# Performance work log

Hardware: AMD Instinct MI355X
Metric: run time of the kernel (lower is better)

## Reference

```python
import jax, jax.numpy as jnp
import numpy as np

N_NODES = 100000
N_EDGES = 1600000
IN_DIM = 64
HID = 64
EDGE_DIM = 1
NUM_GRAPHS = 1000
SCALE = 0.05


def setup_inputs() -> dict:
    key = jax.random.key(0)
    ks = jax.random.split(key, 20)
    x = jax.random.normal(ks[0], (N_NODES, IN_DIM), dtype=jnp.float32)
    edge_index = jax.random.randint(ks[1], (2, N_EDGES), 0, N_NODES, dtype=jnp.int64)
    edge_attr = jax.random.normal(ks[2], (N_EDGES, EDGE_DIM), dtype=jnp.float32)
    batch = jnp.sort(jax.random.randint(ks[3], (N_NODES,), 0, NUM_GRAPHS, dtype=jnp.int64))
    p = lambda k, shp: SCALE * jax.random.normal(k, shp, dtype=jnp.float32)
    return {
        "x": x, "edge_index": edge_index, "edge_attr": edge_attr, "batch": batch,
        # conv1 MLP + edge lin
        "W1a": p(ks[4], (IN_DIM, HID)), "b1a": p(ks[5], (HID,)),
        "W1b": p(ks[6], (HID, HID)), "b1b": p(ks[7], (HID,)),
        "We1": p(ks[8], (EDGE_DIM, IN_DIM)), "be1": p(ks[9], (IN_DIM,)),
        # conv2 MLP + edge lin
        "W2a": p(ks[10], (HID, HID)), "b2a": p(ks[11], (HID,)),
        "W2b": p(ks[12], (HID, HID)), "b2b": p(ks[13], (HID,)),
        "We2": p(ks[14], (EDGE_DIM, HID)), "be2": p(ks[15], (HID,)),
        # classifier
        "Wc1": p(ks[16], (HID, HID)), "bc1": p(ks[17], (HID,)),
        "Wc2": p(ks[18], (HID, 1)), "bc2": p(ks[19], (1,)),
    }


def _gine(x, src, dst, e_proj, Wa, ba, Wb, bb):
    # message: ReLU(x_src + projected edge feature); scatter-sum to target
    msg = jax.nn.relu(x[src] + e_proj)                      # [E, D]
    agg = jax.ops.segment_sum(msg, dst, num_segments=x.shape[0])
    h = x + agg                                             # eps = 0 (default)
    return jax.nn.relu(h @ Wa + ba) @ Wb + bb               # GIN MLP


def reference(x, edge_index, edge_attr, batch,
              W1a, b1a, W1b, b1b, We1, be1,
              W2a, b2a, W2b, b2b, We2, be2,
              Wc1, bc1, Wc2, bc2):
    src, dst = edge_index[0], edge_index[1]
    h = _gine(x, src, dst, edge_attr @ We1 + be1, W1a, b1a, W1b, b1b)
    h = jax.nn.relu(h)  # dropout is identity in eval mode
    h = _gine(h, src, dst, edge_attr @ We2 + be2, W2a, b2a, W2b, b2b)
    h = jax.nn.relu(h)
    # global mean pool over graphs
    sums = jax.ops.segment_sum(h, batch, num_segments=NUM_GRAPHS)
    cnts = jax.ops.segment_sum(jnp.ones((h.shape[0], 1), h.dtype), batch, num_segments=NUM_GRAPHS)
    pooled = sums / jnp.maximum(cnts, 1.0)                  # [G, HID]
    return jax.nn.relu(pooled @ Wc1 + bc1) @ Wc2 + bc2      # [G, 1]
```

## Files before the change

kernel.cpp:

```cpp
#include <hip/hip_runtime.h>

#define N_NODES    100000
#define N_EDGES    1600000
#define DIM        64
#define NUM_GRAPHS 1000
#define CONV_BLK   3125
#define PAD        72

#define SLICES     512
#define SLICE_E    3125
#define NBUCK      782
#define CAP4       3072

typedef __attribute__((ext_vector_type(8))) short bf16x8;
typedef __attribute__((ext_vector_type(4))) float f32x4;

__device__ __forceinline__ unsigned short f2bf(float f) {
    unsigned int b = __float_as_uint(f);
    b += 0x7FFFu + ((b >> 16) & 1u);
    return (unsigned short)(b >> 16);
}

__device__ __forceinline__ float4 ntload_f4(const float* p) {
    f32x4 v = __builtin_nontemporal_load((const f32x4*)p);
    return make_float4(v.x, v.y, v.z, v.w);
}

__global__ __launch_bounds__(256) void prep(
    const int* __restrict__ ei, const float* __restrict__ x,
    int* __restrict__ hist, int* __restrict__ bucketTotal,
    unsigned short* __restrict__ x16)
{
    __shared__ int lh[NBUCK];
    int blk = blockIdx.x, t = threadIdx.x;
    if (blk < SLICES) {
        for (int i = t; i < NBUCK; i += 256) lh[i] = 0;
        __syncthreads();
        const int* dsts = ei + N_EDGES + blk * SLICE_E;
        for (int k = t; k < SLICE_E; k += 256)
            atomicAdd(&lh[dsts[k] >> 7], 1);
        __syncthreads();
        for (int i = t; i < NBUCK; i += 256) {
            int h = lh[i];
            hist[blk * NBUCK + i] = h;
            if (h) atomicAdd(&bucketTotal[i], h);
        }
    } else {
        int tt = (blk - SLICES) * 256 + t;
        if (tt < N_NODES * DIM / 8) {
            int base = tt * 8;
            float4 f0 = ntload_f4(x + base);
            float4 f1 = ntload_f4(x + base + 4);
            uint4 o;
            o.x = (unsigned)f2bf(f0.x) | ((unsigned)f2bf(f0.y) << 16);
            o.y = (unsigned)f2bf(f0.z) | ((unsigned)f2bf(f0.w) << 16);
            o.z = (unsigned)f2bf(f1.x) | ((unsigned)f2bf(f1.y) << 16);
            o.w = (unsigned)f2bf(f1.z) | ((unsigned)f2bf(f1.w) << 16);
            *(uint4*)(x16 + base) = o;
        }
    }
}

__global__ __launch_bounds__(1024) void csr_c2a(
    const int* __restrict__ bucketTotal, int* __restrict__ bucketStart)
{
    __shared__ int sc[1024];
    int t = threadIdx.x;
    int v = (t < NBUCK) ? bucketTotal[t] : 0;
    sc[t] = v;
    __syncthreads();
    for (int o = 1; o < 1024; o <<= 1) {
        int u = (t >= o) ? sc[t - o] : 0;
        __syncthreads();
        sc[t] += u;
        __syncthreads();
    }
    if (t < NBUCK) bucketStart[t] = sc[t] - v;
    if (t == NBUCK - 1) bucketStart[NBUCK] = sc[t];
}

__global__ __launch_bounds__(512) void csr_c2b(
    const int* __restrict__ hist, const int* __restrict__ bucketStart,
    int* __restrict__ off)
{
    __shared__ int sc[512];
    int b = blockIdx.x, t = threadIdx.x;
    int v = hist[t * NBUCK + b];
    sc[t] = v;
    __syncthreads();
    for (int o = 1; o < 512; o <<= 1) {
        int u = (t >= o) ? sc[t - o] : 0;
        __syncthreads();
        sc[t] += u;
        __syncthreads();
    }
    off[b * SLICES + t] = bucketStart[b] + sc[t] - v;
}

__global__ __launch_bounds__(512) void csr_c3(
    const int* __restrict__ ei, const float* __restrict__ ea,
    const int* __restrict__ hist, const int* __restrict__ off,
    int2* __restrict__ tmp)
{
    __shared__ int2 staging[SLICE_E];
    __shared__ int  lstart[NBUCK + 1];
    __shared__ int  garr[NBUCK];
    __shared__ int  lcur[NBUCK];
    __shared__ unsigned short barr[SLICE_E];
    __shared__ int  part[512];

    int s = blockIdx.x, t = threadIdx.x;

    int h[2];
    int mysum = 0;
    #pragma unroll
    for (int j = 0; j < 2; ++j) {
        int b = 2 * t + j;
        h[j] = (b < NBUCK) ? hist[s * NBUCK + b] : 0;
        mysum += h[j];
    }
    part[t] = mysum;
    for (int i = t; i < NBUCK; i += 512) {
        garr[i] = off[i * SLICES + s];
        lcur[i] = 0;
    }
    __syncthreads();
    for (int o = 1; o < 512; o <<= 1) {
        int u = (t >= o) ? part[t - o] : 0;
        __syncthreads();
        part[t] += u;
        __syncthreads();
    }
    int run = part[t] - mysum;
    #pragma unroll
    for (int j = 0; j < 2; ++j) {
        int b = 2 * t + j;
        if (b < NBUCK) lstart[b] = run;
        run += h[j];
    }
    if (t == 0) lstart[NBUCK] = SLICE_E;
    __syncthreads();

    #pragma unroll
    for (int j = 0; j < 2; ++j) {
        int b = 2 * t + j;
        if (b < NBUCK)
            for (int i = lstart[b]; i < lstart[b + 1]; ++i)
                barr[i] = (unsigned short)b;
    }
    __syncthreads();

    for (int k = t; k < SLICE_E; k += 512) {
        int e   = s * SLICE_E + k;
        int src = ei[e];
        int dst = ei[N_EDGES + e];
        float a = ea[e];
        int b   = dst >> 7;
        int p   = lstart[b] + atomicAdd(&lcur[b], 1);
        staging[p] = make_int2(((dst & 127) << 17) | src, __float_as_int(a));
    }
    __syncthreads();

    for (int i = t; i < SLICE_E; i += 512) {
        int b = barr[i];
        tmp[garr[b] + (i - lstart[b])] = staging[i];
    }
}

__global__ __launch_bounds__(512) void csr_c4(
    const int2* __restrict__ tmp, const int* __restrict__ bucketStart,
    int2* __restrict__ csr_e, int* __restrict__ rowptr)
{
    __shared__ int2 staging[CAP4];
    __shared__ int  nh[128];
    __shared__ int  nscan[128];
    __shared__ int  ncur[128];

    int b = blockIdx.x, t = threadIdx.x;
    int lo = bucketStart[b], hi = bucketStart[b + 1];
    int cnt = hi - lo;
    int node0 = b << 7;
    int nn = min(128, N_NODES - node0);

    if (t < 128) { nh[t] = 0; ncur[t] = 0; }
    __syncthreads();

    int2 r[6];
    int nr = 0;
    for (int k = t; k < cnt; k += 512) {
        int2 v = tmp[lo + k];
        r[nr++] = v;
        atomicAdd(&nh[v.x >> 17], 1);
    }
    __syncthreads();

    if (t < 128) nscan[t] = nh[t];
    __syncthreads();
    for (int o = 1; o < 128; o <<= 1) {
        int u = (t >= o && t < 128) ? nscan[t - o] : 0;
        __syncthreads();
        if (t < 128) nscan[t] += u;
        __syncthreads();
    }
    if (t < 128) nscan[t] -= nh[t];
    __syncthreads();

    if (t < nn) rowptr[node0 + t] = lo + nscan[t];
    if (b == NBUCK - 1 && t == 0) rowptr[N_NODES] = N_EDGES;

    for (int k = 0; k < nr; ++k) {
        int dl = r[k].x >> 17;
        int p  = nscan[dl] + atomicAdd(&ncur[dl], 1);
        staging[p] = r[k];
    }
    __syncthreads();

    for (int i = t; i < cnt; i += 512) {
        int2 v = staging[i];
        csr_e[lo + i] = make_int2((v.x & 0x1FFFF) << 4, v.y);
    }
}

template<bool SELF32>
__global__ __launch_bounds__(512, 8) void gine_mfma(
    const uint2* __restrict__ g2,
    const float* __restrict__ self32,
    const int*   __restrict__ rowptr,
    const int2*  __restrict__ csr_e,
    const float* __restrict__ We, const float* __restrict__ be,
    const float* __restrict__ Wa, const float* __restrict__ ba,
    const float* __restrict__ Wb, const float* __restrict__ bb,
    unsigned int* __restrict__ out16)
{
    __shared__ short sWat[64 * PAD];
    __shared__ short sWbt[64 * PAD];
    __shared__ short h16[32 * PAD];
    __shared__ short t16[32 * PAD];

    int t = threadIdx.x;
    for (int i = t; i < 4096; i += 512) {
        int k = i >> 6, n = i & 63;
        sWat[n * PAD + k] = (short)f2bf(Wa[i]);
        sWbt[n * PAD + k] = (short)f2bf(Wb[i]);
    }
    int wave = t >> 6;
    int lane = t & 63;
    int quad = lane >> 4;
    int l15  = lane & 15;
    int slot = wave * 4 + quad;
    int d0   = l15 * 4;
    float4 wp = *(const float4*)(We + d0);
    float4 bp = *(const float4*)(be + d0);
    int mtile = wave & 1;
    int ntile = wave >> 1;
    int col   = ntile * 16 + l15;
    int am    = mtile * 16 + l15;
    float bav = ba[col], bbv = bb[col];
    __syncthreads();

    for (int base = blockIdx.x * 32; base < N_NODES; base += gridDim.x * 32) {
        int  node  = base + slot;
        bool valid = node < N_NODES;
        int beg = 0, deg = 0;
        if (valid) {
            beg = rowptr[node];
            deg = rowptr[node + 1] - beg;
            beg = min(beg, N_EDGES - 1);
        }
        int dm = deg;
        dm = max(dm, __shfl_xor(dm, 16));
        dm = max(dm, __shfl_xor(dm, 32));

        float4 agg = make_float4(0.f, 0.f, 0.f, 0.f);
        #define EDGE4(rr, uu, cond)                                              \
        {                                                                        \
            float s = (cond) ? 1.f : 0.f, av = __int_as_float(rr.y);             \
            float e0 = __uint_as_float(uu.x << 16);                              \
            float e1 = __uint_as_float(uu.x & 0xFFFF0000u);                      \
            float e2 = __uint_as_float(uu.y << 16);                              \
            float e3 = __uint_as_float(uu.y & 0xFFFF0000u);                      \
            agg.x = fmaf(s, fmaxf(e0 + fmaf(av, wp.x, bp.x), 0.f), agg.x);       \
            agg.y = fmaf(s, fmaxf(e1 + fmaf(av, wp.y, bp.y), 0.f), agg.y);       \
            agg.z = fmaf(s, fmaxf(e2 + fmaf(av, wp.z, bp.z), 0.f), agg.z);       \
            agg.w = fmaf(s, fmaxf(e3 + fmaf(av, wp.w, bp.w), 0.f), agg.w);       \
        }
        for (int j = 0; j < dm; j += 4) {
            int2 r0 = csr_e[beg + ((j + 0) < deg ? j + 0 : 0)];
            int2 r1 = csr_e[beg + ((j + 1) < deg ? j + 1 : 0)];
            int2 r2 = csr_e[beg + ((j + 2) < deg ? j + 2 : 0)];
            int2 r3 = csr_e[beg + ((j + 3) < deg ? j + 3 : 0)];
            uint2 u0 = g2[r0.x + l15];
            uint2 u1 = g2[r1.x + l15];
            uint2 u2 = g2[r2.x + l15];
            uint2 u3 = g2[r3.x + l15];
            EDGE4(r0, u0, (j + 0) < deg)
            EDGE4(r1, u1, (j + 1) < deg)
            EDGE4(r2, u2, (j + 2) < deg)
            EDGE4(r3, u3, (j + 3) < deg)
        }
        #undef EDGE4
        if (valid) {
            if (SELF32) {
                float4 sv = *(const float4*)(self32 + (size_t)node * DIM + d0);
                agg.x += sv.x; agg.y += sv.y; agg.z += sv.z; agg.w += sv.w;
            } else {
                uint2 u = g2[node * 16 + l15];
                agg.x += __uint_as_float(u.x << 16);
                agg.y += __uint_as_float(u.x & 0xFFFF0000u);
                agg.z += __uint_as_float(u.y << 16);
                agg.w += __uint_as_float(u.y & 0xFFFF0000u);
            }
        }
        {
            unsigned lo = (unsigned)f2bf(agg.x) | ((unsigned)f2bf(agg.y) << 16);
            unsigned hi = (unsigned)f2bf(agg.z) | ((unsigned)f2bf(agg.w) << 16);
            *(uint2*)&h16[slot * PAD + d0] = make_uint2(lo, hi);
        }
        __syncthreads();

        f32x4 acc = {bav, bav, bav, bav};
        #pragma unroll
        for (int s = 0; s < 2; ++s) {
            bf16x8 a = *(const bf16x8*)&h16[am * PAD + s * 32 + quad * 8];
            bf16x8 b = *(const bf16x8*)&sWat[col * PAD + s * 32 + quad * 8];
            acc = __builtin_amdgcn_mfma_f32_16x16x32_bf16(a, b, acc, 0, 0, 0);
        }
        #pragma unroll
        for (int r = 0; r < 4; ++r) {
            int row = mtile * 16 + quad * 4 + r;
            t16[row * PAD + col] = (short)f2bf(fmaxf(acc[r], 0.f));
        }
        __syncthreads();

        f32x4 acc2 = {bbv, bbv, bbv, bbv};
        #pragma unroll
        for (int s = 0; s < 2; ++s) {
            bf16x8 a = *(const bf16x8*)&t16[am * PAD + s * 32 + quad * 8];
            bf16x8 b = *(const bf16x8*)&sWbt[col * PAD + s * 32 + quad * 8];
            acc2 = __builtin_amdgcn_mfma_f32_16x16x32_bf16(a, b, acc2, 0, 0, 0);
        }
        #pragma unroll
        for (int r = 0; r < 4; ++r) {
            int row = mtile * 16 + quad * 4 + r;
            h16[row * PAD + col] = (short)f2bf(fmaxf(acc2[r], 0.f));
        }
        __syncthreads();
        {
            int nn = t >> 4, dd = (t & 15) * 2;
            if (base + nn < N_NODES) {
                uint2 v = *(const uint2*)&h16[nn * PAD + dd * 2];
                *(uint2*)&out16[(size_t)(base + nn) * 32 + dd] = v;
            }
        }
        __syncthreads();
    }
}

__device__ __forceinline__ int lbound(const int* __restrict__ a, int key) {
    int lo = 0, hi = N_NODES;
    while (lo < hi) {
        int mid = (lo + hi) >> 1;
        if (a[mid] < key) lo = mid + 1; else hi = mid;
    }
    return lo;
}

__global__ __launch_bounds__(256) void pool_cls(
    const unsigned int* __restrict__ B16b,
    const int* __restrict__ batch,
    const float* __restrict__ Wc1,  const float* __restrict__ bc1,
    const float* __restrict__ Wc2,  const float* __restrict__ bc2,
    float* __restrict__ out)
{
    __shared__ float sW[64 * 64];
    __shared__ float sp[4][64];

    int t = threadIdx.x;
    for (int i = t; i < 64 * 64; i += 256) sW[i] = Wc1[i];

    int nl   = t >> 6;
    int lane = t & 63;
    int g    = blockIdx.x * 4 + nl;

    int p = lane & 31, h = lane >> 5;
    if (g < NUM_GRAPHS) {
        int s = lbound(batch, g);
        int e = lbound(batch, g + 1);
        float2 sum = make_float2(0.f, 0.f);
        for (int i = s + h; i < e; i += 2) {
            unsigned u = B16b[(size_t)i * 32 + p];
            sum.x += __uint_as_float(u << 16);
            sum.y += __uint_as_float(u & 0xFFFF0000u);
        }
        sum.x += __shfl_xor(sum.x, 32);
        sum.y += __shfl_xor(sum.y, 32);
        if (h == 0) {
            float inv = 1.f / (float)max(e - s, 1);
            sp[nl][2 * p]     = sum.x * inv;
            sp[nl][2 * p + 1] = sum.y * inv;
        }
    } else if (h == 0) {
        sp[nl][2 * p] = 0.f;
        sp[nl][2 * p + 1] = 0.f;
    }
    __syncthreads();

    float acc = bc1[lane];
    #pragma unroll
    for (int k = 0; k < 64; ++k)
        acc = fmaf(sp[nl][k], sW[k * 64 + lane], acc);
    float tv = fmaxf(acc, 0.f) * Wc2[lane];

    #pragma unroll
    for (int off = 32; off > 0; off >>= 1)
        tv += __shfl_down(tv, off);

    if (lane == 0 && g < NUM_GRAPHS) out[g] = tv + bc2[0];
}

extern "C" void kernel_launch(void* const* d_in, const int* in_sizes, int n_in,
                              void* d_out, int out_size, void* d_ws, size_t ws_size,
                              hipStream_t stream) {
    const float* x     = (const float*)d_in[0];
    const int*   ei    = (const int*)  d_in[1];
    const float* ea    = (const float*)d_in[2];
    const int*   batch = (const int*)  d_in[3];
    const float* W1a = (const float*)d_in[4];
    const float* b1a = (const float*)d_in[5];
    const float* W1b = (const float*)d_in[6];
    const float* b1b = (const float*)d_in[7];
    const float* We1 = (const float*)d_in[8];
    const float* be1 = (const float*)d_in[9];
    const float* W2a = (const float*)d_in[10];
    const float* b2a = (const float*)d_in[11];
    const float* W2b = (const float*)d_in[12];
    const float* b2b = (const float*)d_in[13];
    const float* We2 = (const float*)d_in[14];
    const float* be2 = (const float*)d_in[15];
    const float* Wc1 = (const float*)d_in[16];
    const float* bc1 = (const float*)d_in[17];
    const float* Wc2 = (const float*)d_in[18];
    const float* bc2 = (const float*)d_in[19];

    int2*           csr_e  = (int2*)d_ws;
    unsigned short* x16    = (unsigned short*)(csr_e + N_EDGES);
    unsigned short* B16    = x16 + (size_t)N_NODES * DIM;
    unsigned short* B16b   = B16 + (size_t)N_NODES * DIM;
    int2*           tmp    = (int2*)B16b;
    int*            hist   = (int*)(B16b + (size_t)N_NODES * DIM);
    int*            off    = hist + SLICES * NBUCK;
    int*            bucketTotal = off + NBUCK * SLICES;
    int*            bucketStart = bucketTotal + NBUCK;
    int*            rowptr = bucketStart + (NBUCK + 1);

    hipMemsetAsync(bucketTotal, 0, NBUCK * sizeof(int), stream);

    prep<<<SLICES + CONV_BLK, 256, 0, stream>>>(ei, x, hist, bucketTotal, x16);
    csr_c2a<<<1, 1024, 0, stream>>>(bucketTotal, bucketStart);
    csr_c2b<<<NBUCK, 512, 0, stream>>>(hist, bucketStart, off);
    csr_c3<<<SLICES, 512, 0, stream>>>(ei, ea, hist, off, tmp);
    csr_c4<<<NBUCK, 512, 0, stream>>>(tmp, bucketStart, csr_e, rowptr);

    gine_mfma<true><<<1024, 512, 0, stream>>>(
        (const uint2*)x16, x, rowptr, csr_e,
        We1, be1, W1a, b1a, W1b, b1b, (unsigned int*)B16);

    gine_mfma<false><<<1024, 512, 0, stream>>>(
        (const uint2*)B16, nullptr, rowptr, csr_e,
        We2, be2, W2a, b2a, W2b, b2b, (unsigned int*)B16b);

    pool_cls<<<(NUM_GRAPHS + 3) / 4, 256, 0, stream>>>(
        (const unsigned int*)B16b, batch, Wc1, bc1, Wc2, bc2, (float*)d_out);
}
```

Before: 302.5 us.

## Merge CSR build stages into one cooperative kernel with grid syncs

```diff
diff --git a/kernel.cpp b/kernel.cpp
--- a/kernel.cpp
+++ b/kernel.cpp
@@ -1,10 +1,12 @@
 #include <hip/hip_runtime.h>
+#include <hip/hip_cooperative_groups.h>
+
+namespace cg = cooperative_groups;
 
 #define N_NODES    100000
 #define N_EDGES    1600000
 #define DIM        64
 #define NUM_GRAPHS 1000
-#define CONV_BLK   3125
 #define PAD        72
 
 #define SLICES     512
@@ -26,29 +28,36 @@
     return make_float4(v.x, v.y, v.z, v.w);
 }
 
-__global__ __launch_bounds__(256) void prep(
-    const int* __restrict__ ei, const float* __restrict__ x,
-    int* __restrict__ hist, int* __restrict__ bucketTotal,
-    unsigned short* __restrict__ x16)
+__global__ __launch_bounds__(512, 4) void coop_build(
+    const int* __restrict__ ei, const float* __restrict__ ea,
+    const float* __restrict__ x,
+    int* __restrict__ hist, int* __restrict__ off,
+    int* __restrict__ bucketTotal, int* __restrict__ bucketStart,
+    unsigned short* __restrict__ x16,
+    int2* __restrict__ tmp, int2* __restrict__ csr_e,
+    int* __restrict__ rowptr)
 {
-    __shared__ int lh[NBUCK];
+    cg::grid_group grid = cg::this_grid();
+    __shared__ __align__(16) char smem[42688];
+
     int blk = blockIdx.x, t = threadIdx.x;
-    if (blk < SLICES) {
-        for (int i = t; i < NBUCK; i += 256) lh[i] = 0;
+
+    {
+        int* lh = (int*)smem;
+        for (int i = t; i < NBUCK; i += 512) lh[i] = 0;
         __syncthreads();
         const int* dsts = ei + N_EDGES + blk * SLICE_E;
-        for (int k = t; k < SLICE_E; k += 256)
+        for (int k = t; k < SLICE_E; k += 512)
             atomicAdd(&lh[dsts[k] >> 7], 1);
         __syncthreads();
-        for (int i = t; i < NBUCK; i += 256) {
+        for (int i = t; i < NBUCK; i += 512) {
             int h = lh[i];
             hist[blk * NBUCK + i] = h;
             if (h) atomicAdd(&bucketTotal[i], h);
         }
-    } else {
-        int tt = (blk - SLICES) * 256 + t;
-        if (tt < N_NODES * DIM / 8) {
-            int base = tt * 8;
+        int gid = blk * 512 + t;
+        for (int it = gid; it < N_NODES * DIM / 8; it += 512 * 512) {
+            int base = it * 8;
             float4 f0 = ntload_f4(x + base);
             float4 f1 = ntload_f4(x + base + 4);
             uint4 o;
@@ -59,165 +68,171 @@
             *(uint4*)(x16 + base) = o;
         }
     }
-}
-
-__global__ __launch_bounds__(1024) void csr_c2a(
-    const int* __restrict__ bucketTotal, int* __restrict__ bucketStart)
-{
-    __shared__ int sc[1024];
-    int t = threadIdx.x;
-    int v = (t < NBUCK) ? bucketTotal[t] : 0;
-    sc[t] = v;
-    __syncthreads();
-    for (int o = 1; o < 1024; o <<= 1) {
-        int u = (t >= o) ? sc[t - o] : 0;
-        __syncthreads();
-        sc[t] += u;
-        __syncthreads();
-    }
-    if (t < NBUCK) bucketStart[t] = sc[t] - v;
-    if (t == NBUCK - 1) bucketStart[NBUCK] = sc[t];
-}
-
-__global__ __launch_bounds__(512) void csr_c2b(
-    const int* __restrict__ hist, const int* __restrict__ bucketStart,
-    int* __restrict__ off)
-{
-    __shared__ int sc[512];
-    int b = blockIdx.x, t = threadIdx.x;
-    int v = hist[t * NBUCK + b];
-    sc[t] = v;
-    __syncthreads();
-    for (int o = 1; o < 512; o <<= 1) {
-        int u = (t >= o) ? sc[t - o] : 0;
-        __syncthreads();
-        sc[t] += u;
-        __syncthreads();
-    }
-    off[b * SLICES + t] = bucketStart[b] + sc[t] - v;
-}
-
-__global__ __launch_bounds__(512) void csr_c3(
-    const int* __restrict__ ei, const float* __restrict__ ea,
-    const int* __restrict__ hist, const int* __restrict__ off,
-    int2* __restrict__ tmp)
-{
-    __shared__ int2 staging[SLICE_E];
-    __shared__ int  lstart[NBUCK + 1];
-    __shared__ int  garr[NBUCK];
-    __shared__ int  lcur[NBUCK];
-    __shared__ unsigned short barr[SLICE_E];
-    __shared__ int  part[512];
-
-    int s = blockIdx.x, t = threadIdx.x;
-
-    int h[2];
-    int mysum = 0;
-    #pragma unroll
-    for (int j = 0; j < 2; ++j) {
-        int b = 2 * t + j;
-        h[j] = (b < NBUCK) ? hist[s * NBUCK + b] : 0;
-        mysum += h[j];
-    }
-    part[t] = mysum;
-    for (int i = t; i < NBUCK; i += 512) {
-        garr[i] = off[i * SLICES + s];
-        lcur[i] = 0;
-    }
-    __syncthreads();
-    for (int o = 1; o < 512; o <<= 1) {
-        int u = (t >= o) ? part[t - o] : 0;
-        __syncthreads();
-        part[t] += u;
-        __syncthreads();
-    }
-    int run = part[t] - mysum;
-    #pragma unroll
-    for (int j = 0; j < 2; ++j) {
-        int b = 2 * t + j;
-        if (b < NBUCK) lstart[b] = run;
-        run += h[j];
-    }
-    if (t == 0) lstart[NBUCK] = SLICE_E;
-    __syncthreads();
-
-    #pragma unroll
-    for (int j = 0; j < 2; ++j) {
-        int b = 2 * t + j;
-        if (b < NBUCK)
-            for (int i = lstart[b]; i < lstart[b + 1]; ++i)
-                barr[i] = (unsigned short)b;
-    }
-    __syncthreads();
-
-    for (int k = t; k < SLICE_E; k += 512) {
-        int e   = s * SLICE_E + k;
-        int src = ei[e];
-        int dst = ei[N_EDGES + e];
-        float a = ea[e];
-        int b   = dst >> 7;
-        int p   = lstart[b] + atomicAdd(&lcur[b], 1);
-        staging[p] = make_int2(((dst & 127) << 17) | src, __float_as_int(a));
-    }
-    __syncthreads();
-
-    for (int i = t; i < SLICE_E; i += 512) {
-        int b = barr[i];
-        tmp[garr[b] + (i - lstart[b])] = staging[i];
-    }
-}
-
-__global__ __launch_bounds__(512) void csr_c4(
-    const int2* __restrict__ tmp, const int* __restrict__ bucketStart,
-    int2* __restrict__ csr_e, int* __restrict__ rowptr)
-{
-    __shared__ int2 staging[CAP4];
-    __shared__ int  nh[128];
-    __shared__ int  nscan[128];
-    __shared__ int  ncur[128];
-
-    int b = blockIdx.x, t = threadIdx.x;
-    int lo = bucketStart[b], hi = bucketStart[b + 1];
-    int cnt = hi - lo;
-    int node0 = b << 7;
-    int nn = min(128, N_NODES - node0);
-
-    if (t < 128) { nh[t] = 0; ncur[t] = 0; }
-    __syncthreads();
-
-    int2 r[6];
-    int nr = 0;
-    for (int k = t; k < cnt; k += 512) {
-        int2 v = tmp[lo + k];
-        r[nr++] = v;
-        atomicAdd(&nh[v.x >> 17], 1);
-    }
-    __syncthreads();
-
-    if (t < 128) nscan[t] = nh[t];
-    __syncthreads();
-    for (int o = 1; o < 128; o <<= 1) {
-        int u = (t >= o && t < 128) ? nscan[t - o] : 0;
-        __syncthreads();
-        if (t < 128) nscan[t] += u;
-        __syncthreads();
-    }
-    if (t < 128) nscan[t] -= nh[t];
-    __syncthreads();
-
-    if (t < nn) rowptr[node0 + t] = lo + nscan[t];
-    if (b == NBUCK - 1 && t == 0) rowptr[N_NODES] = N_EDGES;
-
-    for (int k = 0; k < nr; ++k) {
-        int dl = r[k].x >> 17;
-        int p  = nscan[dl] + atomicAdd(&ncur[dl], 1);
-        staging[p] = r[k];
-    }
-    __syncthreads();
-
-    for (int i = t; i < cnt; i += 512) {
-        int2 v = staging[i];
-        csr_e[lo + i] = make_int2((v.x & 0x1FFFF) << 4, v.y);
+    __threadfence();
+    grid.sync();
+
+    if (blk == 0) {
+        int* sc = (int*)smem;
+        int carry = 0;
+        for (int base = 0; base < NBUCK; base += 512) {
+            int idx = base + t;
+            int v = (idx < NBUCK) ? bucketTotal[idx] : 0;
+            sc[t] = v;
+            __syncthreads();
+            for (int o = 1; o < 512; o <<= 1) {
+                int u = (t >= o) ? sc[t - o] : 0;
+                __syncthreads();
+                sc[t] += u;
+                __syncthreads();
+            }
+            if (idx < NBUCK) bucketStart[idx] = carry + sc[t] - v;
+            int tot = sc[511];
+            __syncthreads();
+            carry += tot;
+        }
+        if (t == 0) bucketStart[NBUCK] = carry;
+    }
+    __threadfence();
+    grid.sync();
+
+    {
+        int* sc = (int*)smem;
+        for (int b = blk; b < NBUCK; b += 512) {
+            int v = hist[t * NBUCK + b];
+            sc[t] = v;
+            __syncthreads();
+            for (int o = 1; o < 512; o <<= 1) {
+                int u = (t >= o) ? sc[t - o] : 0;
+                __syncthreads();
+                sc[t] += u;
+                __syncthreads();
+            }
+            off[b * SLICES + t] = bucketStart[b] + sc[t] - v;
+            __syncthreads();
+        }
+    }
+    __threadfence();
+    grid.sync();
+
+    {
+        int2* staging          = (int2*)smem;
+        int*  lstart           = (int*)(smem + 25000);
+        int*  garr             = (int*)(smem + 28132);
+        int*  lcur             = (int*)(smem + 31260);
+        int*  part             = (int*)(smem + 34388);
+        unsigned short* barr   = (unsigned short*)(smem + 36436);
+
+        int s = blk;
+
+        int h[2];
+        int mysum = 0;
+        #pragma unroll
+        for (int j = 0; j < 2; ++j) {
+            int b = 2 * t + j;
+            h[j] = (b < NBUCK) ? hist[s * NBUCK + b] : 0;
+            mysum += h[j];
+        }
+        part[t] = mysum;
+        for (int i = t; i < NBUCK; i += 512) {
+            garr[i] = off[i * SLICES + s];
+            lcur[i] = 0;
+        }
+        __syncthreads();
+        for (int o = 1; o < 512; o <<= 1) {
+            int u = (t >= o) ? part[t - o] : 0;
+            __syncthreads();
+            part[t] += u;
+            __syncthreads();
+        }
+        int run = part[t] - mysum;
+        #pragma unroll
+        for (int j = 0; j < 2; ++j) {
+            int b = 2 * t + j;
+            if (b < NBUCK) lstart[b] = run;
+            run += h[j];
+        }
+        if (t == 0) lstart[NBUCK] = SLICE_E;
+        __syncthreads();
+
+        #pragma unroll
+        for (int j = 0; j < 2; ++j) {
+            int b = 2 * t + j;
+            if (b < NBUCK)
+                for (int i = lstart[b]; i < lstart[b + 1]; ++i)
+                    barr[i] = (unsigned short)b;
+        }
+        __syncthreads();
+
+        for (int k = t; k < SLICE_E; k += 512) {
+            int e   = s * SLICE_E + k;
+            int src = ei[e];
+            int dst = ei[N_EDGES + e];
+            float a = ea[e];
+            int b   = dst >> 7;
+            int p   = lstart[b] + atomicAdd(&lcur[b], 1);
+            staging[p] = make_int2(((dst & 127) << 17) | src, __float_as_int(a));
+        }
+        __syncthreads();
+
+        for (int i = t; i < SLICE_E; i += 512) {
+            int b = barr[i];
+            tmp[garr[b] + (i - lstart[b])] = staging[i];
+        }
+    }
+    __threadfence();
+    grid.sync();
+
+    {
+        int2* staging = (int2*)smem;
+        int*  nh      = (int*)(smem + 24576);
+        int*  nscan   = (int*)(smem + 25088);
+        int*  ncur    = (int*)(smem + 25600);
+
+        for (int b = blk; b < NBUCK; b += 512) {
+            __syncthreads();
+            int lo = bucketStart[b], hi = bucketStart[b + 1];
+            int cnt = hi - lo;
+            int node0 = b << 7;
+            int nn = min(128, N_NODES - node0);
+
+            if (t < 128) { nh[t] = 0; ncur[t] = 0; }
+            __syncthreads();
+
+            int2 r[6];
+            int nr = 0;
+            for (int k = t; k < cnt; k += 512) {
+                int2 v = tmp[lo + k];
+                r[nr++] = v;
+                atomicAdd(&nh[v.x >> 17], 1);
+            }
+            __syncthreads();
+
+            if (t < 128) nscan[t] = nh[t];
+            __syncthreads();
+            for (int o = 1; o < 128; o <<= 1) {
+                int u = (t >= o && t < 128) ? nscan[t - o] : 0;
+                __syncthreads();
+                if (t < 128) nscan[t] += u;
+                __syncthreads();
+            }
+            if (t < 128) nscan[t] -= nh[t];
+            __syncthreads();
+
+            if (t < nn) rowptr[node0 + t] = lo + nscan[t];
+            if (b == NBUCK - 1 && t == 0) rowptr[N_NODES] = N_EDGES;
+
+            for (int k = 0; k < nr; ++k) {
+                int dl = r[k].x >> 17;
+                int p  = nscan[dl] + atomicAdd(&ncur[dl], 1);
+                staging[p] = r[k];
+            }
+            __syncthreads();
+
+            for (int i = t; i < cnt; i += 512) {
+                int2 v = staging[i];
+                csr_e[lo + i] = make_int2((v.x & 0x1FFFF) << 4, v.y);
+            }
+        }
     }
 }
 
@@ -455,11 +470,16 @@
 
     hipMemsetAsync(bucketTotal, 0, NBUCK * sizeof(int), stream);
 
-    prep<<<SLICES + CONV_BLK, 256, 0, stream>>>(ei, x, hist, bucketTotal, x16);
-    csr_c2a<<<1, 1024, 0, stream>>>(bucketTotal, bucketStart);
-    csr_c2b<<<NBUCK, 512, 0, stream>>>(hist, bucketStart, off);
-    csr_c3<<<SLICES, 512, 0, stream>>>(ei, ea, hist, off, tmp);
-    csr_c4<<<NBUCK, 512, 0, stream>>>(tmp, bucketStart, csr_e, rowptr);
+    {
+        void* kargs[] = {
+            (void*)&ei, (void*)&ea, (void*)&x,
+            (void*)&hist, (void*)&off,
+            (void*)&bucketTotal, (void*)&bucketStart,
+            (void*)&x16, (void*)&tmp, (void*)&csr_e, (void*)&rowptr
+        };
+        hipLaunchCooperativeKernel((void*)coop_build, dim3(SLICES), dim3(512),
+                                   kargs, 0, stream);
+    }
 
     gine_mfma<true><<<1024, 512, 0, stream>>>(
         (const uint2*)x16, x, rowptr, csr_e,
```

Result: slower. 866.3 us (+186.4%).

## Fuse final CSR bucket sort with first GINE layer in one kernel

Applied to the files above, without the earlier changes.

```diff
diff --git a/kernel.cpp b/kernel.cpp
--- a/kernel.cpp
+++ b/kernel.cpp
@@ -167,21 +167,39 @@
     }
 }
 
-__global__ __launch_bounds__(512) void csr_c4(
-    const int2* __restrict__ tmp, const int* __restrict__ bucketStart,
-    int2* __restrict__ csr_e, int* __restrict__ rowptr)
+__global__ __launch_bounds__(512, 6) void gine_sort(
+    const uint2* __restrict__ g2,
+    const float* __restrict__ self32,
+    const int*   __restrict__ bucketStart,
+    const int2*  __restrict__ tmp,
+    int2* __restrict__ csr_e,
+    int*  __restrict__ rowptr,
+    const float* __restrict__ We, const float* __restrict__ be,
+    const float* __restrict__ Wa, const float* __restrict__ ba,
+    const float* __restrict__ Wb, const float* __restrict__ bb,
+    unsigned int* __restrict__ out16)
 {
     __shared__ int2 staging[CAP4];
     __shared__ int  nh[128];
     __shared__ int  nscan[128];
     __shared__ int  ncur[128];
-
-    int b = blockIdx.x, t = threadIdx.x;
+    __shared__ short sWat[64 * PAD];
+    __shared__ short sWbt[64 * PAD];
+    __shared__ short h16[32 * PAD];
+    __shared__ short t16[32 * PAD];
+
+    int t = threadIdx.x;
+    int b = blockIdx.x;
     int lo = bucketStart[b], hi = bucketStart[b + 1];
     int cnt = hi - lo;
     int node0 = b << 7;
     int nn = min(128, N_NODES - node0);
 
+    for (int i = t; i < 4096; i += 512) {
+        int k = i >> 6, n = i & 63;
+        sWat[n * PAD + k] = (short)f2bf(Wa[i]);
+        sWbt[n * PAD + k] = (short)f2bf(Wb[i]);
+    }
     if (t < 128) { nh[t] = 0; ncur[t] = 0; }
     __syncthreads();
 
@@ -218,6 +236,108 @@
     for (int i = t; i < cnt; i += 512) {
         int2 v = staging[i];
         csr_e[lo + i] = make_int2((v.x & 0x1FFFF) << 4, v.y);
+    }
+
+    int wave = t >> 6;
+    int lane = t & 63;
+    int quad = lane >> 4;
+    int l15  = lane & 15;
+    int slot = wave * 4 + quad;
+    int d0   = l15 * 4;
+    float4 wp = *(const float4*)(We + d0);
+    float4 bp = *(const float4*)(be + d0);
+    int mtile = wave & 1;
+    int ntile = wave >> 1;
+    int col   = ntile * 16 + l15;
+    int am    = mtile * 16 + l15;
+    float bav = ba[col], bbv = bb[col];
+    int cclamp = max(cnt - 1, 0);
+    __syncthreads();
+
+    for (int g = 0; g < 4; ++g) {
+        int  lrow  = g * 32 + slot;
+        bool valid = lrow < nn;
+        int deg = valid ? nh[lrow] : 0;
+        int beg = valid ? min(nscan[lrow], cclamp) : 0;
+        int dm = deg;
+        dm = max(dm, __shfl_xor(dm, 16));
+        dm = max(dm, __shfl_xor(dm, 32));
+
+        float4 agg = make_float4(0.f, 0.f, 0.f, 0.f);
+        #define EDGE4(rr, uu, cond)                                              \
+        {                                                                        \
+            float s = (cond) ? 1.f : 0.f, av = __int_as_float(rr.y);             \
+            float e0 = __uint_as_float(uu.x << 16);                              \
+            float e1 = __uint_as_float(uu.x & 0xFFFF0000u);                      \
+            float e2 = __uint_as_float(uu.y << 16);                              \
+            float e3 = __uint_as_float(uu.y & 0xFFFF0000u);                      \
+            agg.x = fmaf(s, fmaxf(e0 + fmaf(av, wp.x, bp.x), 0.f), agg.x);       \
+            agg.y = fmaf(s, fmaxf(e1 + fmaf(av, wp.y, bp.y), 0.f), agg.y);       \
+            agg.z = fmaf(s, fmaxf(e2 + fmaf(av, wp.z, bp.z), 0.f), agg.z);       \
+            agg.w = fmaf(s, fmaxf(e3 + fmaf(av, wp.w, bp.w), 0.f), agg.w);       \
+        }
+        for (int j = 0; j < dm; j += 4) {
+            int2 r0 = staging[beg + ((j + 0) < deg ? j + 0 : 0)];
+            int2 r1 = staging[beg + ((j + 1) < deg ? j + 1 : 0)];
+            int2 r2 = staging[beg + ((j + 2) < deg ? j + 2 : 0)];
+            int2 r3 = staging[beg + ((j + 3) < deg ? j + 3 : 0)];
+            uint2 u0 = g2[(r0.x & 0x1FFFF) * 16 + l15];
+            uint2 u1 = g2[(r1.x & 0x1FFFF) * 16 + l15];
+            uint2 u2 = g2[(r2.x & 0x1FFFF) * 16 + l15];
+            uint2 u3 = g2[(r3.x & 0x1FFFF) * 16 + l15];
+            EDGE4(r0, u0, (j + 0) < deg)
+            EDGE4(r1, u1, (j + 1) < deg)
+            EDGE4(r2, u2, (j + 2) < deg)
+            EDGE4(r3, u3, (j + 3) < deg)
+        }
+        #undef EDGE4
+        if (valid) {
+            float4 sv = *(const float4*)(self32 + (size_t)(node0 + lrow) * DIM + d0);
+            agg.x += sv.x; agg.y += sv.y; agg.z += sv.z; agg.w += sv.w;
+        }
+        {
+            unsigned lov = (unsigned)f2bf(agg.x) | ((unsigned)f2bf(agg.y) << 16);
+            unsigned hiv = (unsigned)f2bf(agg.z) | ((unsigned)f2bf(agg.w) << 16);
+            *(uint2*)&h16[slot * PAD + d0] = make_uint2(lov, hiv);
+        }
+        __syncthreads();
+
+        f32x4 acc = {bav, bav, bav, bav};
+        #pragma unroll
+        for (int s = 0; s < 2; ++s) {
+            bf16x8 a = *(const bf16x8*)&h16[am * PAD + s * 32 + quad * 8];
+            bf16x8 bb8 = *(const bf16x8*)&sWat[col * PAD + s * 32 + quad * 8];
+            acc = __builtin_amdgcn_mfma_f32_16x16x32_bf16(a, bb8, acc, 0, 0, 0);
+        }
+        #pragma unroll
+        for (int rr = 0; rr < 4; ++rr) {
+            int row = mtile * 16 + quad * 4 + rr;
+            t16[row * PAD + col] = (short)f2bf(fmaxf(acc[rr], 0.f));
+        }
+        __syncthreads();
+
+        f32x4 acc2 = {bbv, bbv, bbv, bbv};
+        #pragma unroll
+        for (int s = 0; s < 2; ++s) {
+            bf16x8 a = *(const bf16x8*)&t16[am * PAD + s * 32 + quad * 8];
+            bf16x8 bb8 = *(const bf16x8*)&sWbt[col * PAD + s * 32 + quad * 8];
+            acc2 = __builtin_amdgcn_mfma_f32_16x16x32_bf16(a, bb8, acc2, 0, 0, 0);
+        }
+        #pragma unroll
+        for (int rr = 0; rr < 4; ++rr) {
+            int row = mtile * 16 + quad * 4 + rr;
+            h16[row * PAD + col] = (short)f2bf(fmaxf(acc2[rr], 0.f));
+        }
+        __syncthreads();
+        {
+            int n2 = t >> 4, dd = (t & 15) * 2;
+            int lnode = g * 32 + n2;
+            if (node0 + lnode < N_NODES) {
+                uint2 v = *(const uint2*)&h16[n2 * PAD + dd * 2];
+                *(uint2*)&out16[(size_t)(node0 + lnode) * 32 + dd] = v;
+            }
+        }
+        __syncthreads();
     }
 }
 
@@ -459,10 +579,9 @@
     csr_c2a<<<1, 1024, 0, stream>>>(bucketTotal, bucketStart);
     csr_c2b<<<NBUCK, 512, 0, stream>>>(hist, bucketStart, off);
     csr_c3<<<SLICES, 512, 0, stream>>>(ei, ea, hist, off, tmp);
-    csr_c4<<<NBUCK, 512, 0, stream>>>(tmp, bucketStart, csr_e, rowptr);
-
-    gine_mfma<true><<<1024, 512, 0, stream>>>(
-        (const uint2*)x16, x, rowptr, csr_e,
+
+    gine_sort<<<NBUCK, 512, 0, stream>>>(
+        (const uint2*)x16, x, bucketStart, tmp, csr_e, rowptr,
         We1, be1, W1a, b1a, W1b, b1b, (unsigned int*)B16);
 
     gine_mfma<false><<<1024, 512, 0, stream>>>(
```

New measurement: 296.5 us (median of 2 runs). 1.02x faster.
